# Kernel tuning notes

Hardware: AMD Instinct MI355X
Metric: run time of the kernel (lower is better)

Reference implementation:

```python
import jax, jax.numpy as jnp
import numpy as np

B, T, C = 4, 2048, 1024
H, D = 16, 64
EPS = 1.1920929e-07  # torch.finfo(float32).eps, used by F.rms_norm default


def setup_inputs() -> dict:
    key = jax.random.key(0)
    ks = jax.random.split(key, 6)
    x = jax.random.normal(ks[0], (B, T, C), dtype=jnp.float32)
    # rotary cache: theta = 10000^(-2i/D), broadcastable [1, T, 1, D//2]
    inv_freq = 1.0 / (10000.0 ** (jnp.arange(0, D // 2, dtype=jnp.float32) * 2.0 / D))
    ang = jnp.arange(T, dtype=jnp.float32)[:, None] * inv_freq[None, :]  # [T, D//2]
    cos = jnp.cos(ang)[None, :, None, :]
    sin = jnp.sin(ang)[None, :, None, :]
    s = 0.02
    Wq = jax.random.normal(ks[1], (C, C), dtype=jnp.float32) * s
    Wk = jax.random.normal(ks[2], (C, C), dtype=jnp.float32) * s
    Wv = jax.random.normal(ks[3], (C, C), dtype=jnp.float32) * s
    Wo = jax.random.normal(ks[4], (C, C), dtype=jnp.float32) * s
    return {"x": x, "cos": cos, "sin": sin, "Wq": Wq, "Wk": Wk, "Wv": Wv, "Wo": Wo}


def _rope(x, cos, sin):
    d = x.shape[-1] // 2
    x1, x2 = x[..., :d], x[..., d:]
    return jnp.concatenate([x1 * cos + x2 * sin, -x1 * sin + x2 * cos], axis=-1)


def _rmsnorm(x):
    ms = jnp.mean(jnp.square(x), axis=-1, keepdims=True)
    return x * jax.lax.rsqrt(ms + EPS)


def reference(x, cos, sin, Wq, Wk, Wv, Wo):
    Bx, Tx, Cx = x.shape
    q = (x @ Wq.T).reshape(Bx, Tx, H, D)
    k = (x @ Wk.T).reshape(Bx, Tx, H, D)
    v = (x @ Wv.T).reshape(Bx, Tx, H, D)
    q = _rmsnorm(_rope(q, cos, sin))
    k = _rmsnorm(_rope(k, cos, sin))
    scale = 1.0 / jnp.sqrt(jnp.float32(D))
    # non-causal SDPA
    scores = jnp.einsum('bthd,bshd->bhts', q, k) * scale  # [B,H,T,T]
    attn = jax.nn.softmax(scores, axis=-1)
    y = jnp.einsum('bhts,bshd->bthd', attn, v).reshape(Bx, Tx, Cx)
    return y @ Wo.T
```

## Files before the change

### kernel.cpp

```cpp
#include <hip/hip_runtime.h>

#define B_ 4
#define T_ 2048
#define C_ 1024
#define H_ 16
#define D_ 64
#define EPS_ 1.1920929e-07f
#define LOG2E_ 1.4426950408889634f

typedef __attribute__((ext_vector_type(8))) short bf16x8;
typedef __attribute__((ext_vector_type(4))) float f32x4;
typedef __attribute__((ext_vector_type(16))) float f32x16;
typedef unsigned short u16;
typedef unsigned int u32;
typedef __attribute__((ext_vector_type(4))) u32 u32x4;

__device__ inline u16 f2bf(float f) {
  unsigned u = __float_as_uint(f);
  unsigned r = (u + 0x7fffu + ((u >> 16) & 1u)) >> 16;
  return (u16)r;
}

__device__ __forceinline__ void gload16(const void* g, void* l) {
  __builtin_amdgcn_global_load_lds(
      (__attribute__((address_space(1))) void*)g,
      (__attribute__((address_space(3))) void*)l, 16, 0, 0);
}

__global__ __launch_bounds__(256) void cvt_all(const float* __restrict__ x,
                                               const float* __restrict__ wq,
                                               const float* __restrict__ wk,
                                               const float* __restrict__ wv,
                                               const float* __restrict__ wo,
                                               u16* __restrict__ xb,
                                               u16* __restrict__ wqkv,
                                               u16* __restrict__ wob) {
  const int NXB = (int)((size_t)B_ * T_ * C_ / 1024);
  const int WB = (C_ * C_) / 1024;
  const int bid = blockIdx.x;
  const float* src;
  u16* dst;
  int i;
  if (bid < NXB) {
    src = x; dst = xb; i = bid * 1024 + threadIdx.x * 4;
  } else {
    const int wb = bid - NXB;
    const int t = wb / WB;
    const int r = wb - t * WB;
    src = (t == 0) ? wq : (t == 1) ? wk : (t == 2) ? wv : wo;
    dst = (t == 3) ? wob : (wqkv + (size_t)t * (C_ * C_));
    i = r * 1024 + threadIdx.x * 4;
  }
  float4 v = *(const float4*)&src[i];
  ushort4 o;
  o.x = f2bf(v.x); o.y = f2bf(v.y); o.z = f2bf(v.z); o.w = f2bf(v.w);
  *(ushort4*)&dst[i] = o;
}

__global__ __launch_bounds__(512) void gemm_qkv(const u16* __restrict__ X,
                                                const u16* __restrict__ W,
                                                u16* __restrict__ qb,
                                                u16* __restrict__ kb,
                                                u16* __restrict__ vtb,
                                                const float* __restrict__ cs,
                                                const float* __restrict__ sn,
                                                int M, int K) {
  __shared__ short As[2][128 * 64];
  __shared__ short Bs[2][256 * 64];
  const int tid = threadIdx.x;
  const int lane = tid & 63;
  const int wid = tid >> 6;
  const int wm = wid >> 2, wn = wid & 3;
  const int bx = blockIdx.x, by = blockIdx.y;
  const int m0 = by * 128, n0 = bx * 256;
  const int w8 = wid * 8;
  const int lrow = lane >> 3;
  const int scol = ((lane & 7) ^ lrow) * 8;

  f32x4 acc[4][4];
#pragma unroll
  for (int mi = 0; mi < 4; ++mi)
#pragma unroll
    for (int ni = 0; ni < 4; ++ni)
      acc[mi][ni] = (f32x4){0.f, 0.f, 0.f, 0.f};

  const int r = lane & 15;
  const int quad = lane >> 4;
  const int rx = (r & 7) << 3;

#pragma unroll
  for (int ra = 0; ra < 2; ++ra)
    gload16(&X[(size_t)(m0 + ra * 64 + w8 + lrow) * K + scol], &As[0][(ra * 64 + w8) * 64]);
#pragma unroll
  for (int rb = 0; rb < 4; ++rb)
    gload16(&W[(size_t)(n0 + rb * 64 + w8 + lrow) * K + scol], &Bs[0][(rb * 64 + w8) * 64]);
  __syncthreads();

#pragma unroll 2
  for (int it = 0; it < 16; ++it) {
    const int cur = it & 1;
    const int kt = it * 64;
    if (it + 1 < 16) {
      const int nb = cur ^ 1;
#pragma unroll
      for (int ra = 0; ra < 2; ++ra)
        gload16(&X[(size_t)(m0 + ra * 64 + w8 + lrow) * K + kt + 64 + scol], &As[nb][(ra * 64 + w8) * 64]);
#pragma unroll
      for (int rb = 0; rb < 4; ++rb)
        gload16(&W[(size_t)(n0 + rb * 64 + w8 + lrow) * K + kt + 64 + scol], &Bs[nb][(rb * 64 + w8) * 64]);
    }
#pragma unroll
    for (int kc = 0; kc < 2; ++kc) {
      const int ko = (kc * 32 + quad * 8) ^ rx;
      bf16x8 a[4], b[4];
#pragma unroll
      for (int mi = 0; mi < 4; ++mi)
        a[mi] = *(const bf16x8*)&As[cur][(wm * 64 + mi * 16 + r) * 64 + ko];
#pragma unroll
      for (int ni = 0; ni < 4; ++ni)
        b[ni] = *(const bf16x8*)&Bs[cur][(wn * 64 + ni * 16 + r) * 64 + ko];
#pragma unroll
      for (int mi = 0; mi < 4; ++mi)
#pragma unroll
        for (int ni = 0; ni < 4; ++ni)
          acc[mi][ni] = __builtin_amdgcn_mfma_f32_16x16x32_bf16(a[mi], b[ni], acc[mi][ni], 0, 0, 0);
    }
    __syncthreads();
  }

  const int which = bx >> 2;
  const int c0 = (bx & 3) * 256 + wn * 64;

  if (which < 2) {
    u16* dst = (which == 0) ? qb : kb;
#pragma unroll
    for (int mi = 0; mi < 4; ++mi)
#pragma unroll
      for (int j = 0; j < 4; ++j) {
        const int gr = m0 + wm * 64 + mi * 16 + quad * 4 + j;
        const int t = gr & (T_ - 1);
        float o[4];
#pragma unroll
        for (int ni = 0; ni < 2; ++ni) {
          const float c = cs[t * 32 + ni * 16 + r];
          const float s = sn[t * 32 + ni * 16 + r];
          const float x1 = acc[mi][ni][j], x2 = acc[mi][ni + 2][j];
          o[ni]     = x1 * c + x2 * s;
          o[ni + 2] = x2 * c - x1 * s;
        }
        float sq = o[0] * o[0] + o[1] * o[1] + o[2] * o[2] + o[3] * o[3];
        sq += __shfl_xor(sq, 1, 64);
        sq += __shfl_xor(sq, 2, 64);
        sq += __shfl_xor(sq, 4, 64);
        sq += __shfl_xor(sq, 8, 64);
        float rn = rsqrtf(sq * (1.0f / 64.0f) + EPS_);
        if (which == 0) rn *= 0.125f * LOG2E_;
#pragma unroll
        for (int ni = 0; ni < 4; ++ni)
          dst[(size_t)gr * C_ + c0 + ni * 16 + r] = f2bf(o[ni] * rn);
      }
  } else {
    const int h = (bx & 3) * 4 + wn;
    const int gr0 = m0 + wm * 64;
    const int bb = gr0 >> 11;
    const int tbase = gr0 & (T_ - 1);
#pragma unroll
    for (int ni = 0; ni < 4; ++ni) {
      const int d = ni * 16 + r;
      u16* rowp = &vtb[((size_t)((bb * H_ + h) * D_ + d)) * T_ + tbase];
#pragma unroll
      for (int mi = 0; mi < 4; ++mi) {
        u32 lo, hi2;
        asm("v_cvt_pk_bf16_f32 %0, %1, %2" : "=v"(lo) : "v"(acc[mi][ni][0]), "v"(acc[mi][ni][1]));
        asm("v_cvt_pk_bf16_f32 %0, %1, %2" : "=v"(hi2) : "v"(acc[mi][ni][2]), "v"(acc[mi][ni][3]));
        u16* p = rowp + mi * 16 + quad * 2;
        *(u32*)&p[0] = lo;
        *(u32*)&p[8] = hi2;
      }
    }
  }
}

__global__ __launch_bounds__(512) void gemm_out(const u16* __restrict__ X,
                                                const u16* __restrict__ W,
                                                float* __restrict__ Y,
                                                int M, int N, int K) {
  __shared__ short As[2][128 * 64];
  __shared__ short Bs[2][256 * 64];
  const int tid = threadIdx.x;
  const int lane = tid & 63;
  const int wid = tid >> 6;
  const int wm = wid >> 2, wn = wid & 3;
  const int m0 = blockIdx.y * 128, n0 = blockIdx.x * 256;
  const int w8 = wid * 8;
  const int lrow = lane >> 3;
  const int scol = ((lane & 7) ^ lrow) * 8;

  f32x4 acc[4][4];
#pragma unroll
  for (int mi = 0; mi < 4; ++mi)
#pragma unroll
    for (int ni = 0; ni < 4; ++ni)
      acc[mi][ni] = (f32x4){0.f, 0.f, 0.f, 0.f};

  const int r = lane & 15;
  const int quad = lane >> 4;
  const int rx = (r & 7) << 3;

#pragma unroll
  for (int ra = 0; ra < 2; ++ra)
    gload16(&X[(size_t)(m0 + ra * 64 + w8 + lrow) * K + scol], &As[0][(ra * 64 + w8) * 64]);
#pragma unroll
  for (int rb = 0; rb < 4; ++rb)
    gload16(&W[(size_t)(n0 + rb * 64 + w8 + lrow) * K + scol], &Bs[0][(rb * 64 + w8) * 64]);
  __syncthreads();

#pragma unroll 2
  for (int it = 0; it < 16; ++it) {
    const int cur = it & 1;
    const int kt = it * 64;
    if (it + 1 < 16) {
      const int nb = cur ^ 1;
#pragma unroll
      for (int ra = 0; ra < 2; ++ra)
        gload16(&X[(size_t)(m0 + ra * 64 + w8 + lrow) * K + kt + 64 + scol], &As[nb][(ra * 64 + w8) * 64]);
#pragma unroll
      for (int rb = 0; rb < 4; ++rb)
        gload16(&W[(size_t)(n0 + rb * 64 + w8 + lrow) * K + kt + 64 + scol], &Bs[nb][(rb * 64 + w8) * 64]);
    }
#pragma unroll
    for (int kc = 0; kc < 2; ++kc) {
      const int ko = (kc * 32 + quad * 8) ^ rx;
      bf16x8 a[4], b[4];
#pragma unroll
      for (int mi = 0; mi < 4; ++mi)
        a[mi] = *(const bf16x8*)&As[cur][(wm * 64 + mi * 16 + r) * 64 + ko];
#pragma unroll
      for (int ni = 0; ni < 4; ++ni)
        b[ni] = *(const bf16x8*)&Bs[cur][(wn * 64 + ni * 16 + r) * 64 + ko];
#pragma unroll
      for (int mi = 0; mi < 4; ++mi)
#pragma unroll
        for (int ni = 0; ni < 4; ++ni)
          acc[mi][ni] = __builtin_amdgcn_mfma_f32_16x16x32_bf16(a[mi], b[ni], acc[mi][ni], 0, 0, 0);
    }
    __syncthreads();
  }

#pragma unroll
  for (int mi = 0; mi < 4; ++mi)
#pragma unroll
    for (int ni = 0; ni < 4; ++ni) {
      const int gc = n0 + wn * 64 + ni * 16 + r;
#pragma unroll
      for (int j = 0; j < 4; ++j) {
        const int gr = m0 + wm * 64 + mi * 16 + quad * 4 + j;
        Y[(size_t)gr * N + gc] = acc[mi][ni][j];
      }
    }
}

__global__ __launch_bounds__(256) void flash_mfma(const u16* __restrict__ Qb,
                                                  const u16* __restrict__ Kb,
                                                  const u16* __restrict__ Vtb,
                                                  u16* __restrict__ Yb) {
  __shared__ u16 Ks[2][64][72];
  __shared__ u16 Vt[2][64][72];
  const int tid = threadIdx.x;
  const int lane = tid & 63;
  const int w = tid >> 6;
  const int c = lane & 31;
  const int hi = lane >> 5;
  const int bh = blockIdx.x, qt = blockIdx.y;
  const int b = bh >> 4, h = bh & 15;
  const int srow = lane;
  const int sd0 = w * 16;
  const int vrow = tid >> 2;
  const int vco = (tid & 3) * 16;

  const u16* kbase = Kb + ((size_t)(b * T_ + srow) * H_ + h) * D_ + sd0;
  const u16* vbase = Vtb + ((size_t)(bh * 64 + vrow)) * T_ + vco;
  const int KSTRIDE = 64 * H_ * D_;

  bf16x8 k0, k1, v0, v1;
  k0 = *(const bf16x8*)&kbase[0];
  k1 = *(const bf16x8*)&kbase[8];
  v0 = *(const bf16x8*)&vbase[0];
  v1 = *(const bf16x8*)&vbase[8];

  {
    const int row = tid >> 1, half = tid & 1;
    const size_t g = ((size_t)((b * T_ + qt * 128 + row) * H_ + h)) * D_ + half * 32;
    u16* qd = (row < 64) ? &Ks[0][row][half * 32] : &Ks[1][row - 64][half * 32];
    *(bf16x8*)&qd[0]  = *(const bf16x8*)&Qb[g];
    *(bf16x8*)&qd[8]  = *(const bf16x8*)&Qb[g + 8];
    *(bf16x8*)&qd[16] = *(const bf16x8*)&Qb[g + 16];
    *(bf16x8*)&qd[24] = *(const bf16x8*)&Qb[g + 24];
  }
  __syncthreads();
  bf16x8 qf[4];
  {
    const int qr = w * 32 + c;
    const u16* qs = (qr < 64) ? &Ks[0][qr][0] : &Ks[1][qr - 64][0];
#pragma unroll
    for (int ks = 0; ks < 4; ++ks)
      qf[ks] = *(const bf16x8*)&qs[ks * 16 + hi * 8];
  }
  __syncthreads();

  *(bf16x8*)&Ks[0][srow][sd0] = k0;
  *(bf16x8*)&Ks[0][srow][sd0 + 8] = k1;
  *(bf16x8*)&Vt[0][vrow][vco] = v0;
  *(bf16x8*)&Vt[0][vrow][vco + 8] = v1;
  k0 = *(const bf16x8*)&kbase[KSTRIDE];
  k1 = *(const bf16x8*)&kbase[KSTRIDE + 8];
  v0 = *(const bf16x8*)&vbase[64];
  v1 = *(const bf16x8*)&vbase[64 + 8];
  __syncthreads();

  f32x16 oacc[2], oacc_l;
  oacc[0] = (f32x16)(0.f);
  oacc[1] = (f32x16)(0.f);
  oacc_l  = (f32x16)(0.f);
  bf16x8 onesv;
#pragma unroll
  for (int i = 0; i < 8; ++i) onesv[i] = (short)0x3F80;

  const int NT = T_ / 64;
#pragma unroll 2
  for (int t = 0; t < NT; ++t) {
    const int cur = t & 1;

    f32x16 s0 = (f32x16)(0.f), s1 = (f32x16)(0.f);
    __builtin_amdgcn_s_setprio(1);
#pragma unroll
    for (int ks = 0; ks < 4; ++ks) {
      bf16x8 kf0 = *(const bf16x8*)&Ks[cur][c][ks * 16 + hi * 8];
      bf16x8 kf1 = *(const bf16x8*)&Ks[cur][32 + c][ks * 16 + hi * 8];
      s0 = __builtin_amdgcn_mfma_f32_32x32x16_bf16(kf0, qf[ks], s0, 0, 0, 0);
      s1 = __builtin_amdgcn_mfma_f32_32x32x16_bf16(kf1, qf[ks], s1, 0, 0, 0);
    }
    __builtin_amdgcn_s_setprio(0);

    if (t + 1 < NT) {
      const int nxt = cur ^ 1;
      *(bf16x8*)&Ks[nxt][srow][sd0] = k0;
      *(bf16x8*)&Ks[nxt][srow][sd0 + 8] = k1;
      *(bf16x8*)&Vt[nxt][vrow][vco] = v0;
      *(bf16x8*)&Vt[nxt][vrow][vco + 8] = v1;
      if (t + 2 < NT) {
        const int gk = (t + 2) * KSTRIDE;
        k0 = *(const bf16x8*)&kbase[gk];
        k1 = *(const bf16x8*)&kbase[gk + 8];
        const int gv = (t + 2) * 64;
        v0 = *(const bf16x8*)&vbase[gv];
        v1 = *(const bf16x8*)&vbase[gv + 8];
      }
    }

    u32 wrd[2][4][2];
#pragma unroll
    for (int m = 0; m < 4; ++m)
#pragma unroll
      for (int p = 0; p < 2; ++p) {
        float a0 = __builtin_amdgcn_exp2f(s0[m * 4 + p * 2]);
        float a1 = __builtin_amdgcn_exp2f(s0[m * 4 + p * 2 + 1]);
        float b0 = __builtin_amdgcn_exp2f(s1[m * 4 + p * 2]);
        float b1 = __builtin_amdgcn_exp2f(s1[m * 4 + p * 2 + 1]);
        asm("v_cvt_pk_bf16_f32 %0, %1, %2" : "=v"(wrd[0][m][p]) : "v"(a0), "v"(a1));
        asm("v_cvt_pk_bf16_f32 %0, %1, %2" : "=v"(wrd[1][m][p]) : "v"(b0), "v"(b1));
      }
#pragma unroll
    for (int kt2 = 0; kt2 < 2; ++kt2)
#pragma unroll
      for (int m = 0; m < 4; ++m)
        asm("v_permlane32_swap_b32 %0, %1" : "+v"(wrd[kt2][m][0]), "+v"(wrd[kt2][m][1]));

    bf16x8 pa[4];
    pa[0] = __builtin_bit_cast(bf16x8, (u32x4){wrd[0][0][0], wrd[0][0][1], wrd[0][1][0], wrd[0][1][1]});
    pa[1] = __builtin_bit_cast(bf16x8, (u32x4){wrd[0][2][0], wrd[0][2][1], wrd[0][3][0], wrd[0][3][1]});
    pa[2] = __builtin_bit_cast(bf16x8, (u32x4){wrd[1][0][0], wrd[1][0][1], wrd[1][1][0], wrd[1][1][1]});
    pa[3] = __builtin_bit_cast(bf16x8, (u32x4){wrd[1][2][0], wrd[1][2][1], wrd[1][3][0], wrd[1][3][1]});

    __builtin_amdgcn_s_setprio(1);
#pragma unroll
    for (int ks = 0; ks < 4; ++ks) {
      bf16x8 vf0 = *(const bf16x8*)&Vt[cur][c][ks * 16 + hi * 8];
      bf16x8 vf1 = *(const bf16x8*)&Vt[cur][32 + c][ks * 16 + hi * 8];
      oacc[0] = __builtin_amdgcn_mfma_f32_32x32x16_bf16(pa[ks], vf0, oacc[0], 0, 0, 0);
      oacc[1] = __builtin_amdgcn_mfma_f32_32x32x16_bf16(pa[ks], vf1, oacc[1], 0, 0, 0);
      oacc_l  = __builtin_amdgcn_mfma_f32_32x32x16_bf16(pa[ks], onesv, oacc_l, 0, 0, 0);
    }
    __builtin_amdgcn_s_setprio(0);
    __syncthreads();
  }

#pragma unroll
  for (int v = 0; v < 16; ++v) {
    const float inv = 1.0f / oacc_l[v];
    const int q = (v & 3) + 8 * (v >> 2) + 4 * hi;
    const int tq = qt * 128 + w * 32 + q;
    const size_t gbase = ((size_t)((b * T_ + tq) * H_ + h)) * D_;
    Yb[gbase + c]      = f2bf(oacc[0][v] * inv);
    Yb[gbase + 32 + c] = f2bf(oacc[1][v] * inv);
  }
}

extern "C" void kernel_launch(void* const* d_in, const int* in_sizes, int n_in,
                              void* d_out, int out_size, void* d_ws, size_t ws_size,
                              hipStream_t stream) {
  const float* x    = (const float*)d_in[0];
  const float* cosb = (const float*)d_in[1];
  const float* sinb = (const float*)d_in[2];
  const float* Wq   = (const float*)d_in[3];
  const float* Wk   = (const float*)d_in[4];
  const float* Wv   = (const float*)d_in[5];
  const float* Wo   = (const float*)d_in[6];
  float* out = (float*)d_out;

  const size_t NE = (size_t)B_ * T_ * C_;
  const int CC = C_ * C_;
  u16* xb   = (u16*)d_ws;
  u16* qb   = xb + NE;
  u16* kb   = qb + NE;
  u16* vtb  = kb + NE;
  u16* wqkv = vtb + NE;
  u16* wob  = wqkv + 3 * (size_t)CC;
  u16* yb   = xb;

  const int M = B_ * T_;

  const int NXB = (int)(NE / 1024);
  const int NWB = 4 * (CC / 1024);
  cvt_all<<<NXB + NWB, 256, 0, stream>>>(x, Wq, Wk, Wv, Wo, xb, wqkv, wob);

  dim3 qg(12, M / 128), gb(512);
  gemm_qkv<<<qg, gb, 0, stream>>>(xb, wqkv, qb, kb, vtb, cosb, sinb, M, C_);

  dim3 fg(B_ * H_, T_ / 128);
  flash_mfma<<<fg, 256, 0, stream>>>(qb, kb, vtb, yb);

  dim3 og(C_ / 256, M / 128);
  gemm_out<<<og, gb, 0, stream>>>(yb, wob, out, M, C_, C_);
}
```

Baseline: 291.4 us.

## Process 64 query rows per warp in flash attention to reuse K/V fragments

Each warp now handles two 32-row query subtiles, so a block covers 256 queries instead of 128 and each K and V fragment read from shared memory feeds twice as many MFMAs. The S tile is computed in two 32-key halves to bound register pressure, and shared memory is merged into one flat buffer that is reused for Q staging. The grid is halved, which cuts K/V global traffic per query. In exchange, accumulator register use roughly doubles, which may lower occupancy, and there are fewer blocks to spread across CUs.

```diff
diff --git a/kernel.cpp b/kernel.cpp
--- a/kernel.cpp
+++ b/kernel.cpp
@@ -264,8 +264,9 @@
                                                   const u16* __restrict__ Kb,
                                                   const u16* __restrict__ Vtb,
                                                   u16* __restrict__ Yb) {
-  __shared__ u16 Ks[2][64][72];
-  __shared__ u16 Vt[2][64][72];
+  __shared__ u16 sm[4 * 64 * 72];
+#define KSI(buf, rr, cx) ((buf) * 4608 + (rr) * 72 + (cx))
+#define VTI(buf, rr, cx) (9216 + (buf) * 4608 + (rr) * 72 + (cx))
   const int tid = threadIdx.x;
   const int lane = tid & 63;
   const int w = tid >> 6;
@@ -289,39 +290,38 @@
   v1 = *(const bf16x8*)&vbase[8];
 
   {
-    const int row = tid >> 1, half = tid & 1;
-    const size_t g = ((size_t)((b * T_ + qt * 128 + row) * H_ + h)) * D_ + half * 32;
-    u16* qd = (row < 64) ? &Ks[0][row][half * 32] : &Ks[1][row - 64][half * 32];
-    *(bf16x8*)&qd[0]  = *(const bf16x8*)&Qb[g];
-    *(bf16x8*)&qd[8]  = *(const bf16x8*)&Qb[g + 8];
-    *(bf16x8*)&qd[16] = *(const bf16x8*)&Qb[g + 16];
-    *(bf16x8*)&qd[24] = *(const bf16x8*)&Qb[g + 24];
+    const size_t g = ((size_t)((b * T_ + qt * 256 + tid) * H_ + h)) * D_;
+#pragma unroll
+    for (int j = 0; j < 8; ++j)
+      *(bf16x8*)&sm[tid * 68 + j * 8] = *(const bf16x8*)&Qb[g + j * 8];
   }
   __syncthreads();
-  bf16x8 qf[4];
-  {
-    const int qr = w * 32 + c;
-    const u16* qs = (qr < 64) ? &Ks[0][qr][0] : &Ks[1][qr - 64][0];
+  bf16x8 qf[2][4];
+#pragma unroll
+  for (int sub = 0; sub < 2; ++sub)
 #pragma unroll
     for (int ks = 0; ks < 4; ++ks)
-      qf[ks] = *(const bf16x8*)&qs[ks * 16 + hi * 8];
-  }
+      qf[sub][ks] = *(const bf16x8*)&sm[(w * 64 + sub * 32 + c) * 68 + ks * 16 + hi * 8];
   __syncthreads();
 
-  *(bf16x8*)&Ks[0][srow][sd0] = k0;
-  *(bf16x8*)&Ks[0][srow][sd0 + 8] = k1;
-  *(bf16x8*)&Vt[0][vrow][vco] = v0;
-  *(bf16x8*)&Vt[0][vrow][vco + 8] = v1;
+  *(bf16x8*)&sm[KSI(0, srow, sd0)] = k0;
+  *(bf16x8*)&sm[KSI(0, srow, sd0 + 8)] = k1;
+  *(bf16x8*)&sm[VTI(0, vrow, vco)] = v0;
+  *(bf16x8*)&sm[VTI(0, vrow, vco + 8)] = v1;
   k0 = *(const bf16x8*)&kbase[KSTRIDE];
   k1 = *(const bf16x8*)&kbase[KSTRIDE + 8];
   v0 = *(const bf16x8*)&vbase[64];
   v1 = *(const bf16x8*)&vbase[64 + 8];
   __syncthreads();
 
-  f32x16 oacc[2], oacc_l;
-  oacc[0] = (f32x16)(0.f);
-  oacc[1] = (f32x16)(0.f);
-  oacc_l  = (f32x16)(0.f);
+  f32x16 oacc[2][2], lacc[2];
+#pragma unroll
+  for (int sub = 0; sub < 2; ++sub) {
+    oacc[sub][0] = (f32x16)(0.f);
+    oacc[sub][1] = (f32x16)(0.f);
+    lacc[sub] = (f32x16)(0.f);
+  }
+  const f32x16 zro = (f32x16)(0.f);
   bf16x8 onesv;
 #pragma unroll
   for (int i = 0; i < 8; ++i) onesv[i] = (short)0x3F80;
@@ -331,79 +331,93 @@
   for (int t = 0; t < NT; ++t) {
     const int cur = t & 1;
 
-    f32x16 s0 = (f32x16)(0.f), s1 = (f32x16)(0.f);
-    __builtin_amdgcn_s_setprio(1);
-#pragma unroll
-    for (int ks = 0; ks < 4; ++ks) {
-      bf16x8 kf0 = *(const bf16x8*)&Ks[cur][c][ks * 16 + hi * 8];
-      bf16x8 kf1 = *(const bf16x8*)&Ks[cur][32 + c][ks * 16 + hi * 8];
-      s0 = __builtin_amdgcn_mfma_f32_32x32x16_bf16(kf0, qf[ks], s0, 0, 0, 0);
-      s1 = __builtin_amdgcn_mfma_f32_32x32x16_bf16(kf1, qf[ks], s1, 0, 0, 0);
-    }
-    __builtin_amdgcn_s_setprio(0);
-
-    if (t + 1 < NT) {
-      const int nxt = cur ^ 1;
-      *(bf16x8*)&Ks[nxt][srow][sd0] = k0;
-      *(bf16x8*)&Ks[nxt][srow][sd0 + 8] = k1;
-      *(bf16x8*)&Vt[nxt][vrow][vco] = v0;
-      *(bf16x8*)&Vt[nxt][vrow][vco + 8] = v1;
-      if (t + 2 < NT) {
-        const int gk = (t + 2) * KSTRIDE;
-        k0 = *(const bf16x8*)&kbase[gk];
-        k1 = *(const bf16x8*)&kbase[gk + 8];
-        const int gv = (t + 2) * 64;
-        v0 = *(const bf16x8*)&vbase[gv];
-        v1 = *(const bf16x8*)&vbase[gv + 8];
-      }
-    }
-
-    u32 wrd[2][4][2];
-#pragma unroll
-    for (int m = 0; m < 4; ++m)
-#pragma unroll
-      for (int p = 0; p < 2; ++p) {
-        float a0 = __builtin_amdgcn_exp2f(s0[m * 4 + p * 2]);
-        float a1 = __builtin_amdgcn_exp2f(s0[m * 4 + p * 2 + 1]);
-        float b0 = __builtin_amdgcn_exp2f(s1[m * 4 + p * 2]);
-        float b1 = __builtin_amdgcn_exp2f(s1[m * 4 + p * 2 + 1]);
-        asm("v_cvt_pk_bf16_f32 %0, %1, %2" : "=v"(wrd[0][m][p]) : "v"(a0), "v"(a1));
-        asm("v_cvt_pk_bf16_f32 %0, %1, %2" : "=v"(wrd[1][m][p]) : "v"(b0), "v"(b1));
-      }
-#pragma unroll
-    for (int kt2 = 0; kt2 < 2; ++kt2)
-#pragma unroll
-      for (int m = 0; m < 4; ++m)
-        asm("v_permlane32_swap_b32 %0, %1" : "+v"(wrd[kt2][m][0]), "+v"(wrd[kt2][m][1]));
-
-    bf16x8 pa[4];
-    pa[0] = __builtin_bit_cast(bf16x8, (u32x4){wrd[0][0][0], wrd[0][0][1], wrd[0][1][0], wrd[0][1][1]});
-    pa[1] = __builtin_bit_cast(bf16x8, (u32x4){wrd[0][2][0], wrd[0][2][1], wrd[0][3][0], wrd[0][3][1]});
-    pa[2] = __builtin_bit_cast(bf16x8, (u32x4){wrd[1][0][0], wrd[1][0][1], wrd[1][1][0], wrd[1][1][1]});
-    pa[3] = __builtin_bit_cast(bf16x8, (u32x4){wrd[1][2][0], wrd[1][2][1], wrd[1][3][0], wrd[1][3][1]});
-
-    __builtin_amdgcn_s_setprio(1);
-#pragma unroll
-    for (int ks = 0; ks < 4; ++ks) {
-      bf16x8 vf0 = *(const bf16x8*)&Vt[cur][c][ks * 16 + hi * 8];
-      bf16x8 vf1 = *(const bf16x8*)&Vt[cur][32 + c][ks * 16 + hi * 8];
-      oacc[0] = __builtin_amdgcn_mfma_f32_32x32x16_bf16(pa[ks], vf0, oacc[0], 0, 0, 0);
-      oacc[1] = __builtin_amdgcn_mfma_f32_32x32x16_bf16(pa[ks], vf1, oacc[1], 0, 0, 0);
-      oacc_l  = __builtin_amdgcn_mfma_f32_32x32x16_bf16(pa[ks], onesv, oacc_l, 0, 0, 0);
-    }
-    __builtin_amdgcn_s_setprio(0);
+#pragma unroll
+    for (int kh = 0; kh < 2; ++kh) {
+      f32x16 s[2];
+      __builtin_amdgcn_s_setprio(1);
+      {
+        bf16x8 kf = *(const bf16x8*)&sm[KSI(cur, kh * 32 + c, hi * 8)];
+        s[0] = __builtin_amdgcn_mfma_f32_32x32x16_bf16(kf, qf[0][0], zro, 0, 0, 0);
+        s[1] = __builtin_amdgcn_mfma_f32_32x32x16_bf16(kf, qf[1][0], zro, 0, 0, 0);
+      }
+#pragma unroll
+      for (int ks = 1; ks < 4; ++ks) {
+        bf16x8 kf = *(const bf16x8*)&sm[KSI(cur, kh * 32 + c, ks * 16 + hi * 8)];
+        s[0] = __builtin_amdgcn_mfma_f32_32x32x16_bf16(kf, qf[0][ks], s[0], 0, 0, 0);
+        s[1] = __builtin_amdgcn_mfma_f32_32x32x16_bf16(kf, qf[1][ks], s[1], 0, 0, 0);
+      }
+      __builtin_amdgcn_s_setprio(0);
+
+      if (kh == 0 && t + 1 < NT) {
+        const int nxt = cur ^ 1;
+        *(bf16x8*)&sm[KSI(nxt, srow, sd0)] = k0;
+        *(bf16x8*)&sm[KSI(nxt, srow, sd0 + 8)] = k1;
+        *(bf16x8*)&sm[VTI(nxt, vrow, vco)] = v0;
+        *(bf16x8*)&sm[VTI(nxt, vrow, vco + 8)] = v1;
+        if (t + 2 < NT) {
+          const int gk = (t + 2) * KSTRIDE;
+          k0 = *(const bf16x8*)&kbase[gk];
+          k1 = *(const bf16x8*)&kbase[gk + 8];
+          const int gv = (t + 2) * 64;
+          v0 = *(const bf16x8*)&vbase[gv];
+          v1 = *(const bf16x8*)&vbase[gv + 8];
+        }
+      }
+
+      u32 wrd[2][4][2];
+#pragma unroll
+      for (int sub = 0; sub < 2; ++sub)
+#pragma unroll
+        for (int m = 0; m < 4; ++m)
+#pragma unroll
+          for (int p = 0; p < 2; ++p) {
+            float a0 = __builtin_amdgcn_exp2f(s[sub][m * 4 + p * 2]);
+            float a1 = __builtin_amdgcn_exp2f(s[sub][m * 4 + p * 2 + 1]);
+            asm("v_cvt_pk_bf16_f32 %0, %1, %2" : "=v"(wrd[sub][m][p]) : "v"(a0), "v"(a1));
+          }
+#pragma unroll
+      for (int sub = 0; sub < 2; ++sub)
+#pragma unroll
+        for (int m = 0; m < 4; ++m)
+          asm("v_permlane32_swap_b32 %0, %1" : "+v"(wrd[sub][m][0]), "+v"(wrd[sub][m][1]));
+
+      bf16x8 pa[2][2];
+#pragma unroll
+      for (int sub = 0; sub < 2; ++sub) {
+        pa[sub][0] = __builtin_bit_cast(bf16x8, (u32x4){wrd[sub][0][0], wrd[sub][0][1], wrd[sub][1][0], wrd[sub][1][1]});
+        pa[sub][1] = __builtin_bit_cast(bf16x8, (u32x4){wrd[sub][2][0], wrd[sub][2][1], wrd[sub][3][0], wrd[sub][3][1]});
+      }
+
+      __builtin_amdgcn_s_setprio(1);
+#pragma unroll
+      for (int ks2 = 0; ks2 < 2; ++ks2) {
+        bf16x8 vf0 = *(const bf16x8*)&sm[VTI(cur, c, kh * 32 + ks2 * 16 + hi * 8)];
+        bf16x8 vf1 = *(const bf16x8*)&sm[VTI(cur, 32 + c, kh * 32 + ks2 * 16 + hi * 8)];
+        oacc[0][0] = __builtin_amdgcn_mfma_f32_32x32x16_bf16(pa[0][ks2], vf0, oacc[0][0], 0, 0, 0);
+        oacc[0][1] = __builtin_amdgcn_mfma_f32_32x32x16_bf16(pa[0][ks2], vf1, oacc[0][1], 0, 0, 0);
+        oacc[1][0] = __builtin_amdgcn_mfma_f32_32x32x16_bf16(pa[1][ks2], vf0, oacc[1][0], 0, 0, 0);
+        oacc[1][1] = __builtin_amdgcn_mfma_f32_32x32x16_bf16(pa[1][ks2], vf1, oacc[1][1], 0, 0, 0);
+        lacc[0] = __builtin_amdgcn_mfma_f32_32x32x16_bf16(pa[0][ks2], onesv, lacc[0], 0, 0, 0);
+        lacc[1] = __builtin_amdgcn_mfma_f32_32x32x16_bf16(pa[1][ks2], onesv, lacc[1], 0, 0, 0);
+      }
+      __builtin_amdgcn_s_setprio(0);
+    }
     __syncthreads();
   }
 
 #pragma unroll
-  for (int v = 0; v < 16; ++v) {
-    const float inv = 1.0f / oacc_l[v];
-    const int q = (v & 3) + 8 * (v >> 2) + 4 * hi;
-    const int tq = qt * 128 + w * 32 + q;
-    const size_t gbase = ((size_t)((b * T_ + tq) * H_ + h)) * D_;
-    Yb[gbase + c]      = f2bf(oacc[0][v] * inv);
-    Yb[gbase + 32 + c] = f2bf(oacc[1][v] * inv);
-  }
+  for (int sub = 0; sub < 2; ++sub)
+#pragma unroll
+    for (int v = 0; v < 16; ++v) {
+      const float inv = 1.0f / lacc[sub][v];
+      const int q = w * 64 + sub * 32 + (v & 3) + 8 * (v >> 2) + 4 * hi;
+      const int tq = qt * 256 + q;
+      const size_t gbase = ((size_t)((b * T_ + tq) * H_ + h)) * D_;
+      Yb[gbase + c]      = f2bf(oacc[sub][0][v] * inv);
+      Yb[gbase + 32 + c] = f2bf(oacc[sub][1][v] * inv);
+    }
+#undef KSI
+#undef VTI
 }
 
 extern "C" void kernel_launch(void* const* d_in, const int* in_sizes, int n_in,
@@ -437,7 +451,7 @@
   dim3 qg(12, M / 128), gb(512);
   gemm_qkv<<<qg, gb, 0, stream>>>(xb, wqkv, qb, kb, vtb, cosb, sinb, M, C_);
 
-  dim3 fg(B_ * H_, T_ / 128);
+  dim3 fg(B_ * H_, T_ / 256);
   flash_mfma<<<fg, 256, 0, stream>>>(qb, kb, vtb, yb);
 
   dim3 og(C_ / 256, M / 128);
```

Measured after the change: 295.4 us. Within noise of the previous version (+1.3%).
